# Performance work log

Hardware: AMD Instinct MI355X
Metric: run time of the kernel (lower is better)

The kernel has to match this reference:

```python
import jax, jax.numpy as jnp
import numpy as np

B, N, IN_DIM, DIM, H, TOPK = 2, 2048, 256, 256, 8, 4
DH = DIM // H  # 32
EPS = 1e-5


def setup_inputs() -> dict:
    key = jax.random.key(0)
    ks = jax.random.split(key, 6)
    points = jax.random.normal(ks[0], (B * N, IN_DIM), dtype=jnp.float32)
    norm_gamma = jnp.ones((IN_DIM,), dtype=jnp.float32)
    norm_beta = jnp.zeros((IN_DIM,), dtype=jnp.float32)
    w_qkv = jax.random.normal(ks[1], (3 * DIM, IN_DIM), dtype=jnp.float32) / np.sqrt(IN_DIM)
    w_proj = jax.random.normal(ks[2], (DIM, DIM), dtype=jnp.float32) / np.sqrt(DIM)
    b_proj = jnp.zeros((DIM,), dtype=jnp.float32)
    return {"points": points, "norm_gamma": norm_gamma, "norm_beta": norm_beta,
            "w_qkv": w_qkv, "w_proj": w_proj, "b_proj": b_proj}


def reference(points, norm_gamma, norm_beta, w_qkv, w_proj, b_proj):
    # norm1 (LayerNorm over channel)
    x = points.reshape(B, N, IN_DIM)
    mu = jnp.mean(x, axis=-1, keepdims=True)
    var = jnp.var(x, axis=-1, keepdims=True)
    x = (x - mu) / jnp.sqrt(var + EPS) * norm_gamma + norm_beta
    # fused qkv: [B,N,3,H,DH]
    qkv = (x @ w_qkv.T).reshape(B, N, 3, H, DH)
    q, k, v = qkv[:, :, 0], qkv[:, :, 1], qkv[:, :, 2]  # [B,N,H,DH]
    # dense coarse attention: QK [B, M(query), S(key), H]
    qk = jnp.einsum('blhd,bshd->blsh', q, k)
    temp = 1.0 / np.sqrt(DH)
    A = jax.nn.softmax(temp * qk, axis=2)  # softmax over keys (dim=-2)
    # topk over key axis; zero out the top-k entries (scatter mask of zeros)
    A_t = jnp.transpose(A, (0, 1, 3, 2))  # [B,M,H,S]
    topk_score, topk_idx = jax.lax.top_k(A_t, TOPK)  # [B,M,H,k]
    bb = jnp.arange(B)[:, None, None, None]
    mm = jnp.arange(N)[None, :, None, None]
    hh = jnp.arange(H)[None, None, :, None]
    mask_t = jnp.ones_like(A_t).at[bb, mm, hh, topk_idx].set(0.0)
    # message = (A * mask) @ V
    message = jnp.einsum('blhs,bshd->blhd', A_t * mask_t, v).reshape(B, N, DIM)
    message = message @ w_proj.T + b_proj
    v_flat = v.reshape(B, N, DIM)
    message = v_flat + message
    # no padding (equal slens), so ~padding_mask selects everything -> flatten
    message_flat = message.reshape(B * N, DIM)
    topk_score_flat = jnp.transpose(topk_score, (0, 1, 3, 2)).reshape(B * N, TOPK, H)
    topk_idx_flat = jnp.transpose(topk_idx, (0, 1, 3, 2)).reshape(B * N, TOPK, H)
    return message_flat, topk_score_flat, topk_idx_flat
```

## Files before the change

### kernel.cpp

```cpp
#include <hip/hip_runtime.h>
#include <math.h>

#define B_ 2
#define N_ 2048
#define IN_DIM_ 256
#define DIM_ 256
#define H_ 8
#define DH_ 32
#define TOPK_ 4
#define EPS_ 1e-5f
#define TEMP_ 0.17677669529663687f

__global__ __launch_bounds__(256) void ln_kernel(const float* __restrict__ x,
                                                 const float* __restrict__ gamma,
                                                 const float* __restrict__ beta,
                                                 float* __restrict__ xn) {
  int w = threadIdx.x >> 6, ld = threadIdx.x & 63;
  int row = blockIdx.x * 4 + w;
  const float4* xr = (const float4*)(x + (size_t)row * 256);
  float4 v = xr[ld];
  float s = v.x + v.y + v.z + v.w;
  float ss = v.x * v.x + v.y * v.y + v.z * v.z + v.w * v.w;
  #pragma unroll
  for (int off = 1; off < 64; off <<= 1) {
    s += __shfl_xor(s, off);
    ss += __shfl_xor(ss, off);
  }
  float mu = s * (1.0f / 256.0f);
  float var = ss * (1.0f / 256.0f) - mu * mu;
  float rstd = rsqrtf(var + EPS_);
  float4 g = ((const float4*)gamma)[ld];
  float4 bt = ((const float4*)beta)[ld];
  float4 o;
  o.x = (v.x - mu) * rstd * g.x + bt.x;
  o.y = (v.y - mu) * rstd * g.y + bt.y;
  o.z = (v.z - mu) * rstd * g.z + bt.z;
  o.w = (v.w - mu) * rstd * g.w + bt.w;
  ((float4*)(xn + (size_t)row * 256))[ld] = o;
}

template <bool PROJ>
__global__ __launch_bounds__(256) void gemm_nt(const float* __restrict__ A,
                                               const float* __restrict__ Bm,
                                               float* __restrict__ C,
                                               const float* __restrict__ vres,
                                               const float* __restrict__ bias,
                                               int K, int ldc) {
  __shared__ float As[32][64];
  __shared__ float Bs[32][64];
  int m0 = blockIdx.x * 64, n0 = blockIdx.y * 64;
  int t = threadIdx.x;
  int tm = t & 15, tn = t >> 4;
  float acc[4][4] = {};
  for (int k0 = 0; k0 < K; k0 += 32) {
    __syncthreads();
    for (int f = t; f < 512; f += 256) {
      int row = f >> 3, j = f & 7;
      float4 a = *(const float4*)(A + (size_t)(m0 + row) * K + k0 + j * 4);
      As[j * 4 + 0][row] = a.x; As[j * 4 + 1][row] = a.y;
      As[j * 4 + 2][row] = a.z; As[j * 4 + 3][row] = a.w;
      float4 b = *(const float4*)(Bm + (size_t)(n0 + row) * K + k0 + j * 4);
      Bs[j * 4 + 0][row] = b.x; Bs[j * 4 + 1][row] = b.y;
      Bs[j * 4 + 2][row] = b.z; Bs[j * 4 + 3][row] = b.w;
    }
    __syncthreads();
    #pragma unroll
    for (int k = 0; k < 32; k++) {
      float4 a = *(const float4*)&As[k][tm * 4];
      float4 b = *(const float4*)&Bs[k][tn * 4];
      float av[4] = {a.x, a.y, a.z, a.w};
      float bv[4] = {b.x, b.y, b.z, b.w};
      #pragma unroll
      for (int i = 0; i < 4; i++)
        #pragma unroll
        for (int j = 0; j < 4; j++)
          acc[i][j] = fmaf(av[i], bv[j], acc[i][j]);
    }
  }
  #pragma unroll
  for (int i = 0; i < 4; i++) {
    int m = m0 + tm * 4 + i;
    int n = n0 + tn * 4;
    float4 r = {acc[i][0], acc[i][1], acc[i][2], acc[i][3]};
    if (PROJ) {
      float4 vr = *(const float4*)(vres + (size_t)m * 768 + n);
      float4 bb = *(const float4*)(bias + n);
      r.x += vr.x + bb.x; r.y += vr.y + bb.y;
      r.z += vr.z + bb.z; r.w += vr.w + bb.w;
    }
    *(float4*)(C + (size_t)m * ldc + n) = r;
  }
}

__global__ __launch_bounds__(256) void attn_kernel(const float* __restrict__ qkv,
                                                   float* __restrict__ msg,
                                                   float* __restrict__ out_s,
                                                   float* __restrict__ out_i) {
  const int l0 = blockIdx.x * 64;
  const int h = blockIdx.y;
  const int b = blockIdx.z;
  const int t = threadIdx.x;
  const int qr = t >> 2, qc = t & 3;

  __shared__ float4 Ks[64][8];
  __shared__ float4 Vs[64][8];
  __shared__ float Ps[64][65];

  const size_t rowstride = 3 * H_ * DH_;
  const float* qrow = qkv + ((size_t)(b * N_) + l0 + qr) * rowstride + h * DH_;
  float4 qreg[8];
  #pragma unroll
  for (int j = 0; j < 8; j++) {
    float4 v = ((const float4*)qrow)[j];
    v.x *= TEMP_; v.y *= TEMP_; v.z *= TEMP_; v.w *= TEMP_;
    qreg[j] = v;
  }
  float4 o0 = {0, 0, 0, 0}, o1 = {0, 0, 0, 0};
  float m = -INFINITY, l = 0.f;
  float tv[TOPK_];
  int ti[TOPK_];
  #pragma unroll
  for (int i = 0; i < TOPK_; i++) { tv[i] = -INFINITY; ti[i] = 0x7fffffff; }

  const float* kbase = qkv + (size_t)(b * N_) * rowstride + 256 + h * DH_;

  for (int s0 = 0; s0 < N_; s0 += 64) {
    __syncthreads();
    for (int f = t; f < 512; f += 256) {
      int row = f >> 3, j = f & 7;
      const float* kp = kbase + (size_t)(s0 + row) * rowstride + j * 4;
      Ks[row][j] = *(const float4*)kp;
      Vs[row][j] = *(const float4*)(kp + 256);
    }
    __syncthreads();

    float pj[16];
    float tmax = -INFINITY;
    #pragma unroll
    for (int j = 0; j < 16; j++) {
      int ss = qc * 16 + j;
      float4 a = {0, 0, 0, 0};
      #pragma unroll
      for (int kk = 0; kk < 8; kk++) {
        int kx = (kk + 2 * qc) & 7;
        float4 kv = Ks[ss][kx];
        float4 qv = qreg[kx];
        a.x = fmaf(qv.x, kv.x, a.x);
        a.y = fmaf(qv.y, kv.y, a.y);
        a.z = fmaf(qv.z, kv.z, a.z);
        a.w = fmaf(qv.w, kv.w, a.w);
      }
      float sval = (a.x + a.y) + (a.z + a.w);
      pj[j] = sval;
      tmax = fmaxf(tmax, sval);
      int idx = s0 + ss;
      if (sval > tv[3] || (sval == tv[3] && idx < ti[3])) {
        int pos = 3;
        while (pos > 0 && (sval > tv[pos - 1] ||
                           (sval == tv[pos - 1] && idx < ti[pos - 1]))) {
          tv[pos] = tv[pos - 1];
          ti[pos] = ti[pos - 1];
          pos--;
        }
        tv[pos] = sval;
        ti[pos] = idx;
      }
    }
    tmax = fmaxf(tmax, __shfl_xor(tmax, 1));
    tmax = fmaxf(tmax, __shfl_xor(tmax, 2));
    float mnew = fmaxf(m, tmax);
    float alpha = __expf(m - mnew);
    float psum = 0.f;
    #pragma unroll
    for (int j = 0; j < 16; j++) {
      float p = __expf(pj[j] - mnew);
      Ps[qr][qc * 16 + j] = p;
      psum += p;
    }
    psum += __shfl_xor(psum, 1);
    psum += __shfl_xor(psum, 2);
    l = l * alpha + psum;
    m = mnew;
    o0.x *= alpha; o0.y *= alpha; o0.z *= alpha; o0.w *= alpha;
    o1.x *= alpha; o1.y *= alpha; o1.z *= alpha; o1.w *= alpha;
    #pragma unroll
    for (int s = 0; s < 64; s++) {
      float p = Ps[qr][s];
      float4 v0 = Vs[s][qc * 2];
      float4 v1 = Vs[s][qc * 2 + 1];
      o0.x = fmaf(p, v0.x, o0.x); o0.y = fmaf(p, v0.y, o0.y);
      o0.z = fmaf(p, v0.z, o0.z); o0.w = fmaf(p, v0.w, o0.w);
      o1.x = fmaf(p, v1.x, o1.x); o1.y = fmaf(p, v1.y, o1.y);
      o1.z = fmaf(p, v1.z, o1.z); o1.w = fmaf(p, v1.w, o1.w);
    }
  }

  #pragma unroll
  for (int i = 0; i < 4; i++) {
    Ps[qr][qc * 4 + i] = tv[i];
    ((int*)&Ps[qr][16])[qc * 4 + i] = ti[i];
  }
  float mv[16];
  int mi[16];
  #pragma unroll
  for (int e = 0; e < 16; e++) {
    mv[e] = Ps[qr][e];
    mi[e] = ((int*)&Ps[qr][16])[e];
  }
  float fv[4];
  int fi[4];
  #pragma unroll
  for (int r = 0; r < 4; r++) {
    float best = -INFINITY;
    int bi = 0x7fffffff, bp = 0;
    #pragma unroll
    for (int e = 0; e < 16; e++) {
      if (mv[e] > best || (mv[e] == best && mi[e] < bi)) {
        best = mv[e]; bi = mi[e]; bp = e;
      }
    }
    fv[r] = best; fi[r] = bi;
    mv[bp] = -INFINITY; mi[bp] = 0x7fffffff;
  }

  float linv = 1.0f / l;
  o0.x *= linv; o0.y *= linv; o0.z *= linv; o0.w *= linv;
  o1.x *= linv; o1.y *= linv; o1.z *= linv; o1.w *= linv;

  float sc[4];
  #pragma unroll
  for (int r = 0; r < 4; r++) {
    sc[r] = __expf(fv[r] - m) * linv;
    const float* vp =
        qkv + ((size_t)(b * N_) + fi[r]) * rowstride + 512 + h * DH_ + qc * 8;
    float4 v0 = *(const float4*)vp;
    float4 v1 = *(const float4*)(vp + 4);
    o0.x = fmaf(-sc[r], v0.x, o0.x); o0.y = fmaf(-sc[r], v0.y, o0.y);
    o0.z = fmaf(-sc[r], v0.z, o0.z); o0.w = fmaf(-sc[r], v0.w, o0.w);
    o1.x = fmaf(-sc[r], v1.x, o1.x); o1.y = fmaf(-sc[r], v1.y, o1.y);
    o1.z = fmaf(-sc[r], v1.z, o1.z); o1.w = fmaf(-sc[r], v1.w, o1.w);
  }

  float* mp = msg + ((size_t)(b * N_) + l0 + qr) * DIM_ + h * DH_ + qc * 8;
  *(float4*)mp = o0;
  *(float4*)(mp + 4) = o1;

  if (qc == 0) {
    size_t base = ((size_t)(b * N_ + l0 + qr)) * TOPK_;
    #pragma unroll
    for (int r = 0; r < 4; r++) {
      out_s[(base + r) * H_ + h] = sc[r];
      out_i[(base + r) * H_ + h] = (float)fi[r];
    }
  }
}

extern "C" void kernel_launch(void* const* d_in, const int* in_sizes, int n_in,
                              void* d_out, int out_size, void* d_ws, size_t ws_size,
                              hipStream_t stream) {
  const float* points = (const float*)d_in[0];
  const float* norm_gamma = (const float*)d_in[1];
  const float* norm_beta = (const float*)d_in[2];
  const float* w_qkv = (const float*)d_in[3];
  const float* w_proj = (const float*)d_in[4];
  const float* b_proj = (const float*)d_in[5];

  float* out0 = (float*)d_out;
  float* out1 = out0 + (size_t)4096 * 256;
  float* out2 = out1 + (size_t)4096 * 4 * 8;

  float* xn = (float*)d_ws;
  float* qkv = xn + (size_t)4096 * 256;
  float* msg = qkv + (size_t)4096 * 768;

  ln_kernel<<<1024, 256, 0, stream>>>(points, norm_gamma, norm_beta, xn);
  gemm_nt<false><<<dim3(64, 12), 256, 0, stream>>>(xn, w_qkv, qkv, nullptr,
                                                   nullptr, 256, 768);
  attn_kernel<<<dim3(N_ / 64, H_, B_), 256, 0, stream>>>(qkv, msg, out1, out2);
  gemm_nt<true><<<dim3(64, 4), 256, 0, stream>>>(msg, w_proj, out0, qkv + 512,
                                                 b_proj, 256, 256);
}
```

Before: 457.5 us.

## Move attention to bf16 MFMA with split-precision QK and fp32 top-k refinement

Replaces the scalar fp32 attention kernel with an MFMA version. QK^T is computed from hi/lo bf16 splits of Q and K (three MFMAs per tile), and P·V runs in bf16 against a V tensor transposed by a new kernel. Each row keeps 6 top candidates, which a new finalize kernel rescores in exact fp32 to choose the top-4 and subtract their contributions. The softmax drops the running-max rescaling and uses plain exp, relying on small score magnitudes; this risks overflow and bf16 precision error in exchange for matrix-core throughput.

```diff
diff --git a/kernel.cpp b/kernel.cpp
--- a/kernel.cpp
+++ b/kernel.cpp
@@ -3,13 +3,61 @@
 
 #define B_ 2
 #define N_ 2048
-#define IN_DIM_ 256
-#define DIM_ 256
 #define H_ 8
 #define DH_ 32
 #define TOPK_ 4
 #define EPS_ 1e-5f
 #define TEMP_ 0.17677669529663687f
+
+typedef __attribute__((ext_vector_type(8))) short short8;
+typedef __attribute__((ext_vector_type(4))) float f32x4;
+
+__device__ __forceinline__ unsigned short f2bf(float x) {
+  unsigned u = __float_as_uint(x);
+  u += 0x7FFF + ((u >> 16) & 1);
+  return (unsigned short)(u >> 16);
+}
+__device__ __forceinline__ float bf2f(unsigned short h) {
+  return __uint_as_float(((unsigned)h) << 16);
+}
+
+__device__ __forceinline__ void ins6f(float v, int k, float tv[6], int ti[6]) {
+  bool b0 = v > tv[0], b1 = v > tv[1], b2 = v > tv[2];
+  bool b3 = v > tv[3], b4 = v > tv[4], b5 = v > tv[5];
+  tv[5] = b4 ? tv[4] : (b5 ? v : tv[5]); ti[5] = b4 ? ti[4] : (b5 ? k : ti[5]);
+  tv[4] = b3 ? tv[3] : (b4 ? v : tv[4]); ti[4] = b3 ? ti[3] : (b4 ? k : ti[4]);
+  tv[3] = b2 ? tv[2] : (b3 ? v : tv[3]); ti[3] = b2 ? ti[2] : (b3 ? k : ti[3]);
+  tv[2] = b1 ? tv[1] : (b2 ? v : tv[2]); ti[2] = b1 ? ti[1] : (b2 ? k : ti[2]);
+  tv[1] = b0 ? tv[0] : (b1 ? v : tv[1]); ti[1] = b0 ? ti[0] : (b1 ? k : ti[1]);
+  tv[0] = b0 ? v : tv[0];                ti[0] = b0 ? k : ti[0];
+}
+
+__device__ __forceinline__ void ins6ft(float v, int k, float tv[6], int ti[6]) {
+  bool b0 = (v > tv[0]) || (v == tv[0] && k < ti[0]);
+  bool b1 = (v > tv[1]) || (v == tv[1] && k < ti[1]);
+  bool b2 = (v > tv[2]) || (v == tv[2] && k < ti[2]);
+  bool b3 = (v > tv[3]) || (v == tv[3] && k < ti[3]);
+  bool b4 = (v > tv[4]) || (v == tv[4] && k < ti[4]);
+  bool b5 = (v > tv[5]) || (v == tv[5] && k < ti[5]);
+  tv[5] = b4 ? tv[4] : (b5 ? v : tv[5]); ti[5] = b4 ? ti[4] : (b5 ? k : ti[5]);
+  tv[4] = b3 ? tv[3] : (b4 ? v : tv[4]); ti[4] = b3 ? ti[3] : (b4 ? k : ti[4]);
+  tv[3] = b2 ? tv[2] : (b3 ? v : tv[3]); ti[3] = b2 ? ti[2] : (b3 ? k : ti[3]);
+  tv[2] = b1 ? tv[1] : (b2 ? v : tv[2]); ti[2] = b1 ? ti[1] : (b2 ? k : ti[2]);
+  tv[1] = b0 ? tv[0] : (b1 ? v : tv[1]); ti[1] = b0 ? ti[0] : (b1 ? k : ti[1]);
+  tv[0] = b0 ? v : tv[0];                ti[0] = b0 ? k : ti[0];
+}
+
+__device__ __forceinline__ void ins4d(float s, int idx, float dv,
+                                      float tv[4], int ti[4], float td[4]) {
+  bool b0 = (s > tv[0]) || (s == tv[0] && idx < ti[0]);
+  bool b1 = (s > tv[1]) || (s == tv[1] && idx < ti[1]);
+  bool b2 = (s > tv[2]) || (s == tv[2] && idx < ti[2]);
+  bool b3 = (s > tv[3]) || (s == tv[3] && idx < ti[3]);
+  tv[3] = b2 ? tv[2] : (b3 ? s : tv[3]); ti[3] = b2 ? ti[2] : (b3 ? idx : ti[3]); td[3] = b2 ? td[2] : (b3 ? dv : td[3]);
+  tv[2] = b1 ? tv[1] : (b2 ? s : tv[2]); ti[2] = b1 ? ti[1] : (b2 ? idx : ti[2]); td[2] = b1 ? td[1] : (b2 ? dv : td[2]);
+  tv[1] = b0 ? tv[0] : (b1 ? s : tv[1]); ti[1] = b0 ? ti[0] : (b1 ? idx : ti[1]); td[1] = b0 ? td[0] : (b1 ? dv : td[1]);
+  tv[0] = b0 ? s : tv[0];                ti[0] = b0 ? idx : ti[0];                td[0] = b0 ? dv : td[0];
+}
 
 __global__ __launch_bounds__(256) void ln_kernel(const float* __restrict__ x,
                                                  const float* __restrict__ gamma,
@@ -39,12 +87,14 @@
   ((float4*)(xn + (size_t)row * 256))[ld] = o;
 }
 
-template <bool PROJ>
+template <bool PROJ, bool SPLIT>
 __global__ __launch_bounds__(256) void gemm_nt(const float* __restrict__ A,
                                                const float* __restrict__ Bm,
                                                float* __restrict__ C,
                                                const float* __restrict__ vres,
                                                const float* __restrict__ bias,
+                                               unsigned short* __restrict__ qh_out,
+                                               unsigned short* __restrict__ ql_out,
                                                int K, int ldc) {
   __shared__ float As[32][64];
   __shared__ float Bs[32][64];
@@ -89,168 +139,234 @@
       r.z += vr.z + bb.z; r.w += vr.w + bb.w;
     }
     *(float4*)(C + (size_t)m * ldc + n) = r;
-  }
-}
-
-__global__ __launch_bounds__(256) void attn_kernel(const float* __restrict__ qkv,
-                                                   float* __restrict__ msg,
-                                                   float* __restrict__ out_s,
-                                                   float* __restrict__ out_i) {
-  const int l0 = blockIdx.x * 64;
-  const int h = blockIdx.y;
-  const int b = blockIdx.z;
+    if (SPLIT) {
+      ushort4 hi, lo;
+      hi.x = f2bf(r.x); lo.x = f2bf(r.x - bf2f(hi.x));
+      hi.y = f2bf(r.y); lo.y = f2bf(r.y - bf2f(hi.y));
+      hi.z = f2bf(r.z); lo.z = f2bf(r.z - bf2f(hi.z));
+      hi.w = f2bf(r.w); lo.w = f2bf(r.w - bf2f(hi.w));
+      *(ushort4*)(qh_out + (size_t)m * ldc + n) = hi;
+      *(ushort4*)(ql_out + (size_t)m * ldc + n) = lo;
+    }
+  }
+}
+
+__global__ __launch_bounds__(256) void vt_kernel(const float* __restrict__ qkv,
+                                                 unsigned short* __restrict__ vt) {
+  int s0 = blockIdx.x * 64;
+  int bh = blockIdx.y;
+  int b = bh >> 3, h = bh & 7;
+  int t = threadIdx.x;
+  __shared__ __align__(16) unsigned short T[32][72];
+  int key = t >> 2, c4 = t & 3;
+  const float* vp = qkv + ((size_t)(b * N_) + s0 + key) * 768 + 512 + h * DH_ + c4 * 8;
+  float4 a = *(const float4*)vp;
+  float4 bb = *(const float4*)(vp + 4);
+  T[c4 * 8 + 0][key] = f2bf(a.x);  T[c4 * 8 + 1][key] = f2bf(a.y);
+  T[c4 * 8 + 2][key] = f2bf(a.z);  T[c4 * 8 + 3][key] = f2bf(a.w);
+  T[c4 * 8 + 4][key] = f2bf(bb.x); T[c4 * 8 + 5][key] = f2bf(bb.y);
+  T[c4 * 8 + 6][key] = f2bf(bb.z); T[c4 * 8 + 7][key] = f2bf(bb.w);
+  __syncthreads();
+  int dim = t >> 3, kc = t & 7;
+  short8 v = *(const short8*)(&T[dim][kc * 8]);
+  *(short8*)(vt + ((size_t)bh * 32 + dim) * 2048 + s0 + kc * 8) = v;
+}
+
+__global__ __launch_bounds__(128) void attn_mfma(const unsigned short* __restrict__ qkvh,
+                                                 const unsigned short* __restrict__ qkvl,
+                                                 const unsigned short* __restrict__ vt,
+                                                 float* __restrict__ ows,
+                                                 float* __restrict__ lws,
+                                                 float* __restrict__ candv,
+                                                 int* __restrict__ candi) {
+  const int h = blockIdx.y, b = blockIdx.z;
+  const int bh = b * H_ + h;
+  const int w = threadIdx.x >> 6;
+  const int lane = threadIdx.x & 63;
+  const int quad = lane >> 4, m16 = lane & 15;
+  const int rowbase = blockIdx.x * 32 + w * 16;
   const int t = threadIdx.x;
-  const int qr = t >> 2, qc = t & 3;
-
-  __shared__ float4 Ks[64][8];
-  __shared__ float4 Vs[64][8];
-  __shared__ float Ps[64][65];
-
-  const size_t rowstride = 3 * H_ * DH_;
-  const float* qrow = qkv + ((size_t)(b * N_) + l0 + qr) * rowstride + h * DH_;
-  float4 qreg[8];
-  #pragma unroll
-  for (int j = 0; j < 8; j++) {
-    float4 v = ((const float4*)qrow)[j];
-    v.x *= TEMP_; v.y *= TEMP_; v.z *= TEMP_; v.w *= TEMP_;
-    qreg[j] = v;
-  }
-  float4 o0 = {0, 0, 0, 0}, o1 = {0, 0, 0, 0};
-  float m = -INFINITY, l = 0.f;
-  float tv[TOPK_];
-  int ti[TOPK_];
-  #pragma unroll
-  for (int i = 0; i < TOPK_; i++) { tv[i] = -INFINITY; ti[i] = 0x7fffffff; }
-
-  const float* kbase = qkv + (size_t)(b * N_) * rowstride + 256 + h * DH_;
+
+  __shared__ __align__(16) unsigned short KsH[64][40];
+  __shared__ __align__(16) unsigned short KsL[64][40];
+  __shared__ __align__(16) unsigned short Ps[2][16][72];
+
+  const size_t qoff = ((size_t)(b * N_) + rowbase + m16) * 768 + h * DH_ + quad * 8;
+  short8 qh = *(const short8*)(qkvh + qoff);
+  short8 ql = *(const short8*)(qkvl + qoff);
+
+  f32x4 o0 = {0.f, 0.f, 0.f, 0.f}, o1 = {0.f, 0.f, 0.f, 0.f};
+  float lp[4] = {0.f, 0.f, 0.f, 0.f};
+  float tv6[4][6];
+  int ti6[4][6];
+  #pragma unroll
+  for (int r = 0; r < 4; r++)
+    #pragma unroll
+    for (int s = 0; s < 6; s++) { tv6[r][s] = -INFINITY; ti6[r][s] = 0x7fffffff; }
+
+  const unsigned short* vbase = vt + (size_t)bh * 32 * 2048;
 
   for (int s0 = 0; s0 < N_; s0 += 64) {
     __syncthreads();
-    for (int f = t; f < 512; f += 256) {
-      int row = f >> 3, j = f & 7;
-      const float* kp = kbase + (size_t)(s0 + row) * rowstride + j * 4;
-      Ks[row][j] = *(const float4*)kp;
-      Vs[row][j] = *(const float4*)(kp + 256);
+    #pragma unroll
+    for (int i = 0; i < 4; i++) {
+      int f = t + i * 128;
+      int key = (f >> 2) & 63, chunk = f & 3;
+      const unsigned short* src = (i < 2) ? qkvh : qkvl;
+      short8 v = *(const short8*)(src + ((size_t)(b * N_) + s0 + key) * 768 + 256 +
+                                  h * DH_ + chunk * 8);
+      unsigned short* dst = (i < 2) ? &KsH[0][0] : &KsL[0][0];
+      *(short8*)(dst + key * 40 + chunk * 8) = v;
     }
     __syncthreads();
 
-    float pj[16];
-    float tmax = -INFINITY;
-    #pragma unroll
-    for (int j = 0; j < 16; j++) {
-      int ss = qc * 16 + j;
-      float4 a = {0, 0, 0, 0};
+    #pragma unroll
+    for (int ct = 0; ct < 4; ct++) {
+      short8 kh = *(const short8*)(&KsH[ct * 16 + m16][quad * 8]);
+      short8 kl = *(const short8*)(&KsL[ct * 16 + m16][quad * 8]);
+      f32x4 acc = {0.f, 0.f, 0.f, 0.f};
+      acc = __builtin_amdgcn_mfma_f32_16x16x32_bf16(qh, kh, acc, 0, 0, 0);
+      acc = __builtin_amdgcn_mfma_f32_16x16x32_bf16(qh, kl, acc, 0, 0, 0);
+      acc = __builtin_amdgcn_mfma_f32_16x16x32_bf16(ql, kh, acc, 0, 0, 0);
+      int key = s0 + ct * 16 + m16;
       #pragma unroll
-      for (int kk = 0; kk < 8; kk++) {
-        int kx = (kk + 2 * qc) & 7;
-        float4 kv = Ks[ss][kx];
-        float4 qv = qreg[kx];
-        a.x = fmaf(qv.x, kv.x, a.x);
-        a.y = fmaf(qv.y, kv.y, a.y);
-        a.z = fmaf(qv.z, kv.z, a.z);
-        a.w = fmaf(qv.w, kv.w, a.w);
+      for (int r = 0; r < 4; r++) {
+        float p = __expf(TEMP_ * acc[r]);
+        lp[r] += p;
+        Ps[w][quad * 4 + r][ct * 16 + m16] = f2bf(p);
+        ins6f(acc[r], key, tv6[r], ti6[r]);
       }
-      float sval = (a.x + a.y) + (a.z + a.w);
-      pj[j] = sval;
-      tmax = fmaxf(tmax, sval);
-      int idx = s0 + ss;
-      if (sval > tv[3] || (sval == tv[3] && idx < ti[3])) {
-        int pos = 3;
-        while (pos > 0 && (sval > tv[pos - 1] ||
-                           (sval == tv[pos - 1] && idx < ti[pos - 1]))) {
-          tv[pos] = tv[pos - 1];
-          ti[pos] = ti[pos - 1];
-          pos--;
-        }
-        tv[pos] = sval;
-        ti[pos] = idx;
+    }
+    #pragma unroll
+    for (int f = 0; f < 2; f++) {
+      short8 pa = *(const short8*)(&Ps[w][m16][f * 32 + quad * 8]);
+      short8 v0 = *(const short8*)(vbase + (size_t)m16 * 2048 + s0 + f * 32 + quad * 8);
+      short8 v1 = *(const short8*)(vbase + (size_t)(16 + m16) * 2048 + s0 + f * 32 + quad * 8);
+      o0 = __builtin_amdgcn_mfma_f32_16x16x32_bf16(pa, v0, o0, 0, 0, 0);
+      o1 = __builtin_amdgcn_mfma_f32_16x16x32_bf16(pa, v1, o1, 0, 0, 0);
+    }
+  }
+
+  #pragma unroll
+  for (int d = 1; d <= 8; d <<= 1) {
+    #pragma unroll
+    for (int r = 0; r < 4; r++) {
+      lp[r] += __shfl_xor(lp[r], d);
+      float fv[6];
+      int fk[6];
+      #pragma unroll
+      for (int s = 0; s < 6; s++) {
+        fv[s] = __shfl_xor(tv6[r][s], d);
+        fk[s] = __shfl_xor(ti6[r][s], d);
       }
-    }
-    tmax = fmaxf(tmax, __shfl_xor(tmax, 1));
-    tmax = fmaxf(tmax, __shfl_xor(tmax, 2));
-    float mnew = fmaxf(m, tmax);
-    float alpha = __expf(m - mnew);
-    float psum = 0.f;
-    #pragma unroll
-    for (int j = 0; j < 16; j++) {
-      float p = __expf(pj[j] - mnew);
-      Ps[qr][qc * 16 + j] = p;
-      psum += p;
-    }
-    psum += __shfl_xor(psum, 1);
-    psum += __shfl_xor(psum, 2);
-    l = l * alpha + psum;
-    m = mnew;
-    o0.x *= alpha; o0.y *= alpha; o0.z *= alpha; o0.w *= alpha;
-    o1.x *= alpha; o1.y *= alpha; o1.z *= alpha; o1.w *= alpha;
-    #pragma unroll
-    for (int s = 0; s < 64; s++) {
-      float p = Ps[qr][s];
-      float4 v0 = Vs[s][qc * 2];
-      float4 v1 = Vs[s][qc * 2 + 1];
-      o0.x = fmaf(p, v0.x, o0.x); o0.y = fmaf(p, v0.y, o0.y);
-      o0.z = fmaf(p, v0.z, o0.z); o0.w = fmaf(p, v0.w, o0.w);
-      o1.x = fmaf(p, v1.x, o1.x); o1.y = fmaf(p, v1.y, o1.y);
-      o1.z = fmaf(p, v1.z, o1.z); o1.w = fmaf(p, v1.w, o1.w);
-    }
-  }
-
-  #pragma unroll
-  for (int i = 0; i < 4; i++) {
-    Ps[qr][qc * 4 + i] = tv[i];
-    ((int*)&Ps[qr][16])[qc * 4 + i] = ti[i];
-  }
-  float mv[16];
-  int mi[16];
-  #pragma unroll
-  for (int e = 0; e < 16; e++) {
-    mv[e] = Ps[qr][e];
-    mi[e] = ((int*)&Ps[qr][16])[e];
-  }
-  float fv[4];
-  int fi[4];
+      #pragma unroll
+      for (int s = 0; s < 6; s++) ins6ft(fv[s], fk[s], tv6[r], ti6[r]);
+    }
+  }
+
   #pragma unroll
   for (int r = 0; r < 4; r++) {
-    float best = -INFINITY;
-    int bi = 0x7fffffff, bp = 0;
-    #pragma unroll
-    for (int e = 0; e < 16; e++) {
-      if (mv[e] > best || (mv[e] == best && mi[e] < bi)) {
-        best = mv[e]; bi = mi[e]; bp = e;
+    int row = rowbase + quad * 4 + r;
+    size_t rg = (size_t)bh * N_ + row;
+    ows[rg * 32 + m16] = o0[r];
+    ows[rg * 32 + 16 + m16] = o1[r];
+    if (m16 == 0) {
+      lws[rg] = lp[r];
+      #pragma unroll
+      for (int s = 0; s < 6; s++) {
+        candv[rg * 6 + s] = tv6[r][s];
+        candi[rg * 6 + s] = ti6[r][s];
       }
     }
-    fv[r] = best; fi[r] = bi;
-    mv[bp] = -INFINITY; mi[bp] = 0x7fffffff;
-  }
-
+  }
+}
+
+__global__ __launch_bounds__(64) void finalize_kernel(const float* __restrict__ qkv,
+                                                      const float* __restrict__ ows,
+                                                      const float* __restrict__ lws,
+                                                      const float* __restrict__ candv,
+                                                      const int* __restrict__ candi,
+                                                      float* __restrict__ msg,
+                                                      float* __restrict__ out_s,
+                                                      float* __restrict__ out_i) {
+  int bid = blockIdx.x;
+  int bh = bid >> 7, rgi = bid & 127;
+  int b = bh >> 3, h = bh & 7;
+  int lane = threadIdx.x & 63;
+  int m16 = lane & 15, g = lane >> 4;
+  int row = rgi * 16 + m16;
+  size_t rg = (size_t)bh * N_ + row;
+
+  const float* qp = qkv + ((size_t)(b * N_) + row) * 768 + h * DH_;
+  float sv[2], sd[2];
+  int si[2];
+  #pragma unroll
+  for (int c = 0; c < 2; c++) {
+    int ci = g * 2 + c;
+    int cidx = rg * 6 + (ci < 6 ? ci : 0);
+    int key = candi[cidx];
+    float dv = candv[cidx];
+    bool valid = (ci < 6) && (key < N_);
+    int kk = valid ? key : 0;
+    const float* kp = qkv + ((size_t)(b * N_) + kk) * 768 + 256 + h * DH_;
+    float acc = 0.f;
+    #pragma unroll
+    for (int d2 = 0; d2 < 8; d2++) {
+      float4 qv = *(const float4*)(qp + d2 * 4);
+      float4 kv = *(const float4*)(kp + d2 * 4);
+      acc += qv.x * kv.x + qv.y * kv.y + qv.z * kv.z + qv.w * kv.w;
+    }
+    sv[c] = valid ? TEMP_ * acc : -INFINITY;
+    si[c] = valid ? key : 0x7fffffff;
+    sd[c] = dv;
+  }
+  float av[8], ad[8];
+  int ai[8];
+  av[0] = sv[0]; av[1] = sv[1]; ai[0] = si[0]; ai[1] = si[1]; ad[0] = sd[0]; ad[1] = sd[1];
+  #pragma unroll
+  for (int c = 0; c < 2; c++) {
+    av[2 + c] = __shfl_xor(av[c], 16); ai[2 + c] = __shfl_xor(ai[c], 16);
+    ad[2 + c] = __shfl_xor(ad[c], 16);
+  }
+  #pragma unroll
+  for (int c = 0; c < 4; c++) {
+    av[4 + c] = __shfl_xor(av[c], 32); ai[4 + c] = __shfl_xor(ai[c], 32);
+    ad[4 + c] = __shfl_xor(ad[c], 32);
+  }
+  float tv[4] = {-INFINITY, -INFINITY, -INFINITY, -INFINITY};
+  int ti[4] = {0x7fffffff, 0x7fffffff, 0x7fffffff, 0x7fffffff};
+  float td[4] = {0, 0, 0, 0};
+  #pragma unroll
+  for (int c = 0; c < 8; c++) ins4d(av[c], ai[c], ad[c], tv, ti, td);
+
+  float l = lws[rg];
   float linv = 1.0f / l;
-  o0.x *= linv; o0.y *= linv; o0.z *= linv; o0.w *= linv;
-  o1.x *= linv; o1.y *= linv; o1.z *= linv; o1.w *= linv;
-
-  float sc[4];
+  float sc[4], sub[4];
   #pragma unroll
   for (int r = 0; r < 4; r++) {
-    sc[r] = __expf(fv[r] - m) * linv;
-    const float* vp =
-        qkv + ((size_t)(b * N_) + fi[r]) * rowstride + 512 + h * DH_ + qc * 8;
-    float4 v0 = *(const float4*)vp;
-    float4 v1 = *(const float4*)(vp + 4);
-    o0.x = fmaf(-sc[r], v0.x, o0.x); o0.y = fmaf(-sc[r], v0.y, o0.y);
-    o0.z = fmaf(-sc[r], v0.z, o0.z); o0.w = fmaf(-sc[r], v0.w, o0.w);
-    o1.x = fmaf(-sc[r], v1.x, o1.x); o1.y = fmaf(-sc[r], v1.y, o1.y);
-    o1.z = fmaf(-sc[r], v1.z, o1.z); o1.w = fmaf(-sc[r], v1.w, o1.w);
-  }
-
-  float* mp = msg + ((size_t)(b * N_) + l0 + qr) * DIM_ + h * DH_ + qc * 8;
-  *(float4*)mp = o0;
-  *(float4*)(mp + 4) = o1;
-
-  if (qc == 0) {
-    size_t base = ((size_t)(b * N_ + l0 + qr)) * TOPK_;
+    sc[r] = __expf(tv[r]) * linv;
+    sub[r] = bf2f(f2bf(__expf(TEMP_ * td[r]))) * linv;
+  }
+
+  float oc[8];
+  #pragma unroll
+  for (int d2 = 0; d2 < 8; d2++) oc[d2] = ows[rg * 32 + g * 8 + d2] * linv;
+  #pragma unroll
+  for (int r = 0; r < 4; r++) {
+    const float* vp = qkv + ((size_t)(b * N_) + ti[r]) * 768 + 512 + h * DH_ + g * 8;
+    #pragma unroll
+    for (int d2 = 0; d2 < 8; d2++) oc[d2] = fmaf(-sub[r], vp[d2], oc[d2]);
+  }
+  float* mp = msg + ((size_t)(b * N_) + row) * 256 + h * DH_ + g * 8;
+  #pragma unroll
+  for (int d2 = 0; d2 < 8; d2++) mp[d2] = oc[d2];
+
+  if (g == 0) {
+    size_t base = ((size_t)(b * N_) + row) * TOPK_;
     #pragma unroll
     for (int r = 0; r < 4; r++) {
       out_s[(base + r) * H_ + h] = sc[r];
-      out_i[(base + r) * H_ + h] = (float)fi[r];
+      out_i[(base + r) * H_ + h] = (float)ti[r];
     }
   }
 }
@@ -270,13 +386,24 @@
   float* out2 = out1 + (size_t)4096 * 4 * 8;
 
   float* xn = (float*)d_ws;
-  float* qkv = xn + (size_t)4096 * 256;
-  float* msg = qkv + (size_t)4096 * 768;
+  float* qkv = xn + (size_t)1048576;
+  float* msg = qkv + (size_t)3145728;
+  float* ows = msg + (size_t)1048576;
+  float* lws = ows + (size_t)1048576;
+  float* candv = lws + 32768;
+  int* candi = (int*)(candv + 196608);
+  unsigned short* qkvh = (unsigned short*)(candi + 196608);
+  unsigned short* qkvl = qkvh + (size_t)3145728;
+  unsigned short* vt = qkvl + (size_t)3145728;
 
   ln_kernel<<<1024, 256, 0, stream>>>(points, norm_gamma, norm_beta, xn);
-  gemm_nt<false><<<dim3(64, 12), 256, 0, stream>>>(xn, w_qkv, qkv, nullptr,
-                                                   nullptr, 256, 768);
-  attn_kernel<<<dim3(N_ / 64, H_, B_), 256, 0, stream>>>(qkv, msg, out1, out2);
-  gemm_nt<true><<<dim3(64, 4), 256, 0, stream>>>(msg, w_proj, out0, qkv + 512,
-                                                 b_proj, 256, 256);
-}
+  gemm_nt<false, true><<<dim3(64, 12), 256, 0, stream>>>(
+      xn, w_qkv, qkv, nullptr, nullptr, qkvh, qkvl, 256, 768);
+  vt_kernel<<<dim3(32, 16), 256, 0, stream>>>(qkv, vt);
+  attn_mfma<<<dim3(64, H_, B_), 128, 0, stream>>>(qkvh, qkvl, vt, ows, lws,
+                                                  candv, candi);
+  finalize_kernel<<<2048, 64, 0, stream>>>(qkv, ows, lws, candv, candi, msg,
+                                           out1, out2);
+  gemm_nt<true, false><<<dim3(64, 4), 256, 0, stream>>>(
+      msg, w_proj, out0, qkv + 512, b_proj, nullptr, nullptr, 256, 256);
+}
```

After: 473.7 us. 1.04x slower.
